# Kernel tuning notes

Measured on AMD Instinct MI355X. Metric: run time of the kernel, lower is better.

The kernel has to match this reference:

```python
import jax, jax.numpy as jnp
import numpy as np

B, T, D, H, L, DFF, MAXLEN = 4, 2048, 512, 8, 6, 2048, 2048
DK = D // H
SCALE = float(1.0 / np.sqrt(DK * 2))  # 1/sqrt(d_k*2)


def layer_norm(x, g, b, eps=1e-5):
    m = jnp.mean(x, axis=-1, keepdims=True)
    v = jnp.var(x, axis=-1, keepdims=True)
    return (x - m) / jnp.sqrt(v + eps) * g + b


def setup_inputs() -> dict:
    key = jax.random.key(0)
    it = iter(jax.random.split(key, 48))
    def n(shape, std=0.02):
        return jax.random.normal(next(it), shape, dtype=jnp.float32) * std
    inp = {}
    inp['x'] = jax.random.normal(next(it), (B, T), dtype=jnp.float32)
    inp['ip_w'] = n((1, D)); inp['ip_b'] = jnp.zeros((D,))
    inp['ip_ln_g'] = jnp.ones((D,)); inp['ip_ln_b'] = jnp.zeros((D,))
    inp['pos_embed'] = n((MAXLEN, D), 0.01)
    inp['pad_token'] = n((D,), 0.01)
    inp['Wq'] = n((L, D, D)); inp['bq'] = jnp.zeros((L, D))
    inp['Wk'] = n((L, D, D)); inp['bk'] = jnp.zeros((L, D))
    inp['Wv'] = n((L, D, D)); inp['bv'] = jnp.zeros((L, D))
    inp['Wo'] = n((L, D, D)); inp['bo'] = jnp.zeros((L, D))
    inp['ln1_g'] = jnp.ones((L, D)); inp['ln1_b'] = jnp.zeros((L, D))
    inp['ln2_g'] = jnp.ones((L, D)); inp['ln2_b'] = jnp.zeros((L, D))
    inp['W1'] = n((L, D, DFF)); inp['b1'] = jnp.zeros((L, DFF))
    inp['W2'] = n((L, DFF, D)); inp['b2'] = jnp.zeros((L, D))
    inp['gate1'] = jnp.full((L,), 0.1); inp['gate2'] = jnp.full((L,), 0.1)
    inp['fn_g'] = jnp.ones((D,)); inp['fn_b'] = jnp.zeros((D,))
    for p in ['bh', 'ah', 'ch']:
        inp[p + '_ln_g'] = jnp.ones((D,)); inp[p + '_ln_b'] = jnp.zeros((D,))
    inp['bh_w'] = n((D, 2), 0.01); inp['bh_b'] = jnp.zeros((2,))
    inp['ah_w'] = n((D, 1), 0.01); inp['ah_b'] = jnp.zeros((1,))
    inp['ch_w'] = n((D, 1), 0.01); inp['ch_b'] = jnp.zeros((1,))
    return inp


def _forward(x, ip_w, ip_b, ip_ln_g, ip_ln_b, pos_embed, pad_token,
             Wq, bq, Wk, bk, Wv, bv, Wo, bo,
             ln1_g, ln1_b, ln2_g, ln2_b, W1, b1, W2, b2, gate1, gate2,
             fn_g, fn_b, bh_ln_g, bh_ln_b, bh_w, bh_b,
             ah_ln_g, ah_ln_b, ah_w, ah_b, ch_ln_g, ch_ln_b, ch_w, ch_b):
    Bx, Tx = x.shape
    xc = jnp.clip(x, -10.0, 10.0)
    pad_mask = xc == -1.0  # [B,T]
    h = layer_norm(xc[..., None] @ ip_w + ip_b, ip_ln_g, ip_ln_b)  # [B,T,D]
    h = h + 0.1 * pos_embed[None, :Tx, :]
    h = jnp.where(pad_mask[..., None], pad_token, h)
    cmask = jnp.triu(jnp.full((Tx, Tx), -10000.0, dtype=h.dtype), k=1)  # additive causal mask
    for i in range(L):
        xn = layer_norm(h, ln1_g[i], ln1_b[i])
        def heads(w, b, xn=xn):
            return (xn @ w + b).reshape(Bx, Tx, H, DK).transpose(0, 2, 1, 3)
        q = heads(Wq[i], bq[i]); k = heads(Wk[i], bk[i]); v = heads(Wv[i], bv[i])
        q = q / jnp.maximum(jnp.linalg.norm(q, axis=-1, keepdims=True), 1e-8)
        k = k / jnp.maximum(jnp.linalg.norm(k, axis=-1, keepdims=True), 1e-8)
        scores = jnp.clip(jnp.einsum('bhtd,bhsd->bhts', q, k) * SCALE, -5.0, 5.0) + cmask
        a = jax.nn.softmax(scores / 1.5, axis=-1)
        o = jnp.einsum('bhts,bhsd->bhtd', a, v).transpose(0, 2, 1, 3).reshape(Bx, Tx, D)
        h = h + gate1[i] * ((o @ Wo[i] + bo[i]) * 0.5)
        xn2 = layer_norm(h, ln2_g[i], ln2_b[i])
        ffn = jax.nn.gelu(xn2 @ W1[i] + b1[i], approximate=False) @ W2[i] + b2[i]
        h = jnp.clip(h + gate2[i] * ffn, -10.0, 10.0)
    h = layer_norm(h, fn_g, fn_b)
    m = (~pad_mask).astype(h.dtype)[..., None]
    mean = (h * m).sum(axis=1) / jnp.maximum(m.sum(axis=1), 1.0)  # masked mean pool [B,D]
    binary = layer_norm(mean, bh_ln_g, bh_ln_b) @ bh_w + bh_b
    anomaly = layer_norm(mean, ah_ln_g, ah_ln_b) @ ah_w + ah_b
    caustic = jax.nn.sigmoid(layer_norm(mean, ch_ln_g, ch_ln_b) @ ch_w + ch_b)
    return jnp.concatenate([binary, anomaly, caustic], axis=-1)  # [B,4]


def reference(x, ip_w, ip_b, ip_ln_g, ip_ln_b, pos_embed, pad_token,
              Wq, bq, Wk, bk, Wv, bv, Wo, bo,
              ln1_g, ln1_b, ln2_g, ln2_b, W1, b1, W2, b2, gate1, gate2,
              fn_g, fn_b, bh_ln_g, bh_ln_b, bh_w, bh_b,
              ah_ln_g, ah_ln_b, ah_w, ah_b, ch_ln_g, ch_ln_b, ch_w, ch_b):
    return _forward(x, ip_w, ip_b, ip_ln_g, ip_ln_b, pos_embed, pad_token,
                    Wq, bq, Wk, bk, Wv, bv, Wo, bo,
                    ln1_g, ln1_b, ln2_g, ln2_b, W1, b1, W2, b2, gate1, gate2,
                    fn_g, fn_b, bh_ln_g, bh_ln_b, bh_w, bh_b,
                    ah_ln_g, ah_ln_b, ah_w, ah_b, ch_ln_g, ch_ln_b, ch_w, ch_b)
```

## Files before the change

kernel.cpp:

```cpp
#include <hip/hip_runtime.h>
#include <hip/hip_bf16.h>
#include <math.h>

constexpr int Bsz = 4, T = 2048, D = 512, H = 8, Lnum = 6, DFF = 2048, DK = 64;
constexpr int QS2 = 1024;
constexpr float K2 = 0.08838834764831845f / 1.5f;

typedef __attribute__((ext_vector_type(8))) short svec8;
typedef __attribute__((ext_vector_type(4))) float fvec4;

__device__ __forceinline__ fvec4 mfma16(svec8 a, svec8 b, fvec4 c) {
    return __builtin_amdgcn_mfma_f32_16x16x32_bf16(a, b, c, 0, 0, 0);
}
__device__ __forceinline__ unsigned short f2b(float f) {
    unsigned int u = __float_as_uint(f);
    u += 0x7fffu + ((u >> 16) & 1u);
    return (unsigned short)(u >> 16);
}
__device__ __forceinline__ unsigned int pk2b(float a, float b) {
    __hip_bfloat162 h = __float22bfloat162_rn(float2{a, b});
    return *(unsigned int*)&h;
}
__device__ __forceinline__ float wave_red_sum(float v) {
    for (int o = 32; o > 0; o >>= 1) v += __shfl_down(v, o, 64);
    return __shfl(v, 0, 64);
}
__device__ __forceinline__ void glds16(const unsigned short* g, unsigned short* l) {
    __builtin_amdgcn_global_load_lds(
        (const __attribute__((address_space(1))) unsigned int*)g,
        (__attribute__((address_space(3))) unsigned int*)l, 16, 0, 0);
}
#define FRAG(buf, row, kq) (*(const svec8*)((buf) + (((row) << 6) | ((((kq) ^ ((row) & 7))) << 3))))

__global__ __launch_bounds__(64)
void embed_kernel(const float* __restrict__ x, const float* __restrict__ ip_w,
                  const float* __restrict__ ip_b, const float* __restrict__ g,
                  const float* __restrict__ bta, const float* __restrict__ pos,
                  const float* __restrict__ pad_tok, float* __restrict__ h)
{
    int row = blockIdx.x;
    int t = row & (T - 1);
    int lane = threadIdx.x;
    float xv = x[row];
    float xc = fminf(fmaxf(xv, -10.f), 10.f);
    bool pad = (xc == -1.0f);
    float pre[8];
    float s = 0.f, s2 = 0.f;
#pragma unroll
    for (int j = 0; j < 8; j++) {
        int d = j * 64 + lane;
        float p = xc * ip_w[d] + ip_b[d];
        pre[j] = p; s += p; s2 += p * p;
    }
    s = wave_red_sum(s); s2 = wave_red_sum(s2);
    float m = s * (1.f / 512.f);
    float var = s2 * (1.f / 512.f) - m * m;
    float rstd = 1.f / sqrtf(var + 1e-5f);
#pragma unroll
    for (int j = 0; j < 8; j++) {
        int d = j * 64 + lane;
        float hv = (pre[j] - m) * rstd * g[d] + bta[d] + 0.1f * pos[(size_t)t * D + d];
        if (pad) hv = pad_tok[d];
        h[(size_t)row * D + d] = hv;
    }
}

__global__ __launch_bounds__(256)
void ln_kernel(const float* __restrict__ in, float* __restrict__ out,
               const float* __restrict__ g, const float* __restrict__ b)
{
    int row = blockIdx.x * 4 + (threadIdx.x >> 6);
    int lane = threadIdx.x & 63;
    const float* r = in + (size_t)row * D;
    float4 v0 = ((const float4*)r)[lane];
    float4 v1 = ((const float4*)r)[lane + 64];
    float s = v0.x + v0.y + v0.z + v0.w + v1.x + v1.y + v1.z + v1.w;
    float s2 = v0.x*v0.x + v0.y*v0.y + v0.z*v0.z + v0.w*v0.w
             + v1.x*v1.x + v1.y*v1.y + v1.z*v1.z + v1.w*v1.w;
    s = wave_red_sum(s); s2 = wave_red_sum(s2);
    float m = s * (1.f / 512.f);
    float var = s2 * (1.f / 512.f) - m * m;
    float rstd = 1.f / sqrtf(var + 1e-5f);
    float4 g0 = ((const float4*)g)[lane], g1 = ((const float4*)g)[lane + 64];
    float4 b0 = ((const float4*)b)[lane], b1 = ((const float4*)b)[lane + 64];
    float4 o0, o1;
    o0.x = (v0.x - m) * rstd * g0.x + b0.x; o0.y = (v0.y - m) * rstd * g0.y + b0.y;
    o0.z = (v0.z - m) * rstd * g0.z + b0.z; o0.w = (v0.w - m) * rstd * g0.w + b0.w;
    o1.x = (v1.x - m) * rstd * g1.x + b1.x; o1.y = (v1.y - m) * rstd * g1.y + b1.y;
    o1.z = (v1.z - m) * rstd * g1.z + b1.z; o1.w = (v1.w - m) * rstd * g1.w + b1.w;
    ((float4*)(out + (size_t)row * D))[lane] = o0;
    ((float4*)(out + (size_t)row * D))[lane + 64] = o1;
}

__device__ __forceinline__ void ln_row_bf16(const float* __restrict__ in, unsigned short* __restrict__ out,
                                            const float* __restrict__ g, const float* __restrict__ b,
                                            int row, int lane)
{
    const float* r = in + (size_t)row * D;
    float4 v0 = ((const float4*)r)[lane];
    float4 v1 = ((const float4*)r)[lane + 64];
    float s = v0.x + v0.y + v0.z + v0.w + v1.x + v1.y + v1.z + v1.w;
    float s2 = v0.x*v0.x + v0.y*v0.y + v0.z*v0.z + v0.w*v0.w
             + v1.x*v1.x + v1.y*v1.y + v1.z*v1.z + v1.w*v1.w;
    s = wave_red_sum(s); s2 = wave_red_sum(s2);
    float m = s * (1.f / 512.f);
    float var = s2 * (1.f / 512.f) - m * m;
    float rstd = 1.f / sqrtf(var + 1e-5f);
    float4 g0 = ((const float4*)g)[lane], g1 = ((const float4*)g)[lane + 64];
    float4 b0 = ((const float4*)b)[lane], b1 = ((const float4*)b)[lane + 64];
    unsigned short o0[4], o1[4];
    o0[0] = f2b((v0.x - m) * rstd * g0.x + b0.x); o0[1] = f2b((v0.y - m) * rstd * g0.y + b0.y);
    o0[2] = f2b((v0.z - m) * rstd * g0.z + b0.z); o0[3] = f2b((v0.w - m) * rstd * g0.w + b0.w);
    o1[0] = f2b((v1.x - m) * rstd * g1.x + b1.x); o1[1] = f2b((v1.y - m) * rstd * g1.y + b1.y);
    o1[2] = f2b((v1.z - m) * rstd * g1.z + b1.z); o1[3] = f2b((v1.w - m) * rstd * g1.w + b1.w);
    *(uint2*)(out + (size_t)row * D + lane * 4) = *(uint2*)o0;
    *(uint2*)(out + (size_t)row * D + 256 + lane * 4) = *(uint2*)o1;
}

__global__ __launch_bounds__(256)
void ln_bf16_kernel(const float* __restrict__ in, unsigned short* __restrict__ out,
                    const float* __restrict__ g, const float* __restrict__ b)
{
    ln_row_bf16(in, out, g, b, blockIdx.x * 4 + (threadIdx.x >> 6), threadIdx.x & 63);
}

__global__ __launch_bounds__(256)
void prep_kernel(const float* __restrict__ wq, const float* __restrict__ wk,
                 const float* __restrict__ wv, const float* __restrict__ wo,
                 const float* __restrict__ w1, const float* __restrict__ w2,
                 unsigned short* __restrict__ oq, unsigned short* __restrict__ ok,
                 unsigned short* __restrict__ ov, unsigned short* __restrict__ oo,
                 unsigned short* __restrict__ o1, unsigned short* __restrict__ o2,
                 const float* __restrict__ hin, unsigned short* __restrict__ lnout,
                 const float* __restrict__ ln_g, const float* __restrict__ ln_b)
{
    __shared__ float tile[32][33];
    int bid = blockIdx.x;
    if (bid >= 3072) {
        int row = (bid - 3072) * 4 + (threadIdx.x >> 6);
        ln_row_bf16(hin, lnout, ln_g, ln_b, row, threadIdx.x & 63);
        return;
    }
    const float* in; unsigned short* out; int K, N, kt, nt;
    if (bid < 1024) {
        int sel = bid >> 8, loc = bid & 255;
        in  = sel == 0 ? wq : sel == 1 ? wk : sel == 2 ? wv : wo;
        out = sel == 0 ? oq : sel == 1 ? ok : sel == 2 ? ov : oo;
        K = 512; N = 512; kt = loc >> 4; nt = loc & 15;
    } else if (bid < 2048) {
        int loc = bid - 1024; in = w1; out = o1; K = 512; N = 2048; kt = loc >> 6; nt = loc & 63;
    } else {
        int loc = bid - 2048; in = w2; out = o2; K = 2048; N = 512; kt = loc >> 4; nt = loc & 15;
    }
    int k0 = kt * 32, n0 = nt * 32;
    int t = threadIdx.x;
    int kr = t >> 3, nc = (t & 7) * 4;
    float4 v = *(const float4*)(in + (size_t)(k0 + kr) * N + n0 + nc);
    tile[kr][nc] = v.x; tile[kr][nc + 1] = v.y; tile[kr][nc + 2] = v.z; tile[kr][nc + 3] = v.w;
    __syncthreads();
    unsigned short o[4];
#pragma unroll
    for (int i = 0; i < 4; i++) o[i] = f2b(tile[nc + i][kr]);
    *(uint2*)(out + (size_t)(n0 + kr) * K + k0 + nc) = *(uint2*)o;
}

template<int EPI, int OBF, int BM>
__global__ __launch_bounds__(256)
void gemm_bf16(const unsigned short* __restrict__ A, const unsigned short* __restrict__ BT,
               const float* __restrict__ bias, const float* __restrict__ bias_b,
               const float* __restrict__ bias_c, const float* __restrict__ res,
               void* __restrict__ Cv, unsigned short* __restrict__ vtout,
               int M, int N, int K, const float* __restrict__ gate_p)
{
    constexpr int WN = (BM == 128) ? 2 : 4;
    constexpr int WSPAN = 128 / WN;
    constexpr int NT = WSPAN / 16;
    constexpr int MT = 4;
    constexpr int ACALLS = BM / 32;
    constexpr int SMEMSZ = (EPI == 0) ? 17408 : (BM * 64 + 128 * 64);
    __shared__ __align__(16) unsigned short SMEM[SMEMSZ];
    unsigned short* As = SMEM;
    unsigned short* Bs = SMEM + BM * 64;
    const int tid = threadIdx.x, w = tid >> 6, lane = tid & 63, quad = lane >> 4, ln = lane & 15;
    const int wm = w / WN, wn = w % WN;
    const int m0 = blockIdx.x * BM, n0 = blockIdx.y * 128;
    const int jg = (lane & 7) ^ ((lane >> 3) & 7);
    const int rb = w * 8 + (lane >> 3);
    const unsigned short* Agl = A + (size_t)(m0 + rb) * K + jg * 8;
    const unsigned short* Bgl = BT + (size_t)(n0 + rb) * K + jg * 8;

    fvec4 acc[MT][NT];
#pragma unroll
    for (int mt = 0; mt < MT; mt++)
#pragma unroll
        for (int nt = 0; nt < NT; nt++)
#pragma unroll
            for (int r = 0; r < 4; r++) acc[mt][nt][r] = 0.f;

    for (int k0 = 0; k0 < K; k0 += 64) {
        __syncthreads();
#pragma unroll
        for (int c = 0; c < ACALLS; c++)
            glds16(Agl + k0 + (size_t)c * 32 * K, As + c * 2048 + w * 512);
#pragma unroll
        for (int c = 0; c < 4; c++)
            glds16(Bgl + k0 + (size_t)c * 32 * K, Bs + c * 2048 + w * 512);
        __syncthreads();
#pragma unroll
        for (int kk = 0; kk < 2; kk++) {
            svec8 af[MT], bfr[NT];
#pragma unroll
            for (int mt = 0; mt < MT; mt++)
                af[mt] = FRAG(As, wm * 64 + mt * 16 + ln, kk * 4 + quad);
#pragma unroll
            for (int nt = 0; nt < NT; nt++)
                bfr[nt] = FRAG(Bs, wn * WSPAN + nt * 16 + ln, kk * 4 + quad);
#pragma unroll
            for (int mt = 0; mt < MT; mt++)
#pragma unroll
                for (int nt = 0; nt < NT; nt++)
                    acc[mt][nt] = mfma16(af[mt], bfr[nt], acc[mt][nt]);
        }
    }

    const float gate = (EPI == 1 || EPI == 3) ? gate_p[0] : 0.f;
    float bb[NT];
#pragma unroll
    for (int nt = 0; nt < NT; nt++) {
        int n = n0 + wn * WSPAN + nt * 16 + ln;
        if (EPI == 0) {
            int nseg = n >> 9;
            const float* bsel = nseg == 0 ? bias : (nseg == 1 ? bias_b : bias_c);
            bb[nt] = bsel[n - nseg * 512];
        } else {
            bb[nt] = bias[n];
        }
    }

    if (EPI == 0 && n0 >= 1024) {
        __syncthreads();
#pragma unroll
        for (int mt = 0; mt < MT; mt++) {
#pragma unroll
            for (int nt = 0; nt < NT; nt++) {
                int nl = wn * 64 + nt * 16 + ln;
                int mb = wm * 64 + mt * 16 + quad * 4;
                unsigned int lo = pk2b(acc[mt][nt][0] + bb[nt], acc[mt][nt][1] + bb[nt]);
                unsigned int hi = pk2b(acc[mt][nt][2] + bb[nt], acc[mt][nt][3] + bb[nt]);
                uint2 u; u.x = lo; u.y = hi;
                *(uint2*)(SMEM + nl * 136 + mb) = u;
            }
        }
        __syncthreads();
        int row = tid >> 1, half = (tid & 1) * 64;
        unsigned short* dst = vtout + ((size_t)((m0 >> 11) * 512 + (n0 - 1024) + row)) * T
                              + (m0 & (T - 1)) + half;
        const unsigned short* src = SMEM + row * 136 + half;
#pragma unroll
        for (int j = 0; j < 8; j++) *(uint4*)(dst + j * 8) = *(const uint4*)(src + j * 8);
        return;
    }

#pragma unroll
    for (int mt = 0; mt < MT; mt++) {
        float v[NT][4];
#pragma unroll
        for (int nt = 0; nt < NT; nt++)
#pragma unroll
            for (int r = 0; r < 4; r++) v[nt][r] = acc[mt][nt][r] + bb[nt];
        if (EPI == 0) {
            const float fac = ((n0 + wn * WSPAN) < 512) ? K2 : 1.f;
#pragma unroll
            for (int r = 0; r < 4; r++) {
                float s = 0.f;
#pragma unroll
                for (int nt = 0; nt < NT; nt++) s += v[nt][r] * v[nt][r];
                s += __shfl_xor(s, 1); s += __shfl_xor(s, 2);
                s += __shfl_xor(s, 4); s += __shfl_xor(s, 8);
                float rs = fac / fmaxf(sqrtf(s), 1e-8f);
#pragma unroll
                for (int nt = 0; nt < NT; nt++) v[nt][r] *= rs;
            }
        }
#pragma unroll
        for (int nt = 0; nt < NT; nt++) {
            int n = n0 + wn * WSPAN + nt * 16 + ln;
#pragma unroll
            for (int r = 0; r < 4; r++) {
                int m = m0 + wm * 64 + mt * 16 + quad * 4 + r;
                float val = v[nt][r];
                if (EPI == 0) {
                    ((unsigned short*)Cv)[(size_t)m * QS2 + n] = f2b(val);
                } else {
                    size_t off = (size_t)m * N + n;
                    if (EPI == 1) val = res[off] + gate * 0.5f * val;
                    else if (EPI == 2) {
                        float u = val;
                        float z = 0.7978845608028654f * fmaf(0.044715f * u, u * u, u);
                        float e = __builtin_amdgcn_exp2f(z * 2.8853900817779268f);
                        float rr = __builtin_amdgcn_rcpf(e + 1.f);
                        val = u * (1.f - rr);
                    }
                    else if (EPI == 3) val = fminf(fmaxf(res[off] + gate * val, -10.f), 10.f);
                    if (OBF) ((unsigned short*)Cv)[off] = f2b(val);
                    else ((float*)Cv)[off] = val;
                }
            }
        }
    }
}

template<bool MERGED, bool DIAGS>
__device__ __forceinline__ void attn_step2(
    unsigned short* PsA, unsigned short* PsB,
    const unsigned short* Ks, const unsigned short* Vt,
    svec8 qA0, svec8 qA1, svec8 qB0, svec8 qB1,
    bool diagA, bool diagB,
    fvec4 (&oA)[4], fvec4& lA, fvec4 (&oB)[4], fvec4& lB,
    int w, int quad, int ln)
{
    constexpr short BONE = (short)0x3F80;
    const svec8 ONES8 = {BONE, BONE, BONE, BONE, BONE, BONE, BONE, BONE};
    const int qrow = w * 16 + ln;
    const int prow_base = (qrow << 6);
#pragma unroll
    for (int nt = 0; nt < 4; nt++) {
        svec8 kf0 = FRAG(Ks, nt * 16 + ln, quad);
        svec8 kf1 = FRAG(Ks, nt * 16 + ln, 4 + quad);
        const int sbase = nt * 16 + quad * 4;
        const int paddr = prow_base | ((((sbase >> 3) ^ (qrow & 7))) << 3) | (sbase & 7);
        {
            fvec4 z; z[0] = z[1] = z[2] = z[3] = 0.f;
            z = mfma16(kf0, qB0, z);
            z = mfma16(kf1, qB1, z);
            float p[4];
#pragma unroll
            for (int r = 0; r < 4; r++) {
                float y = z[r];
                float pv = fmaf(y, fmaf(y, 0.5f, 1.f), 1.f);
                if (DIAGS && diagB && (sbase + r > qrow)) pv = 0.f;
                p[r] = pv;
            }
            uint2 u; u.x = pk2b(p[0], p[1]); u.y = pk2b(p[2], p[3]);
            *(uint2*)(PsB + paddr) = u;
        }
        if (MERGED) {
            fvec4 z; z[0] = z[1] = z[2] = z[3] = 0.f;
            z = mfma16(kf0, qA0, z);
            z = mfma16(kf1, qA1, z);
            float p[4];
#pragma unroll
            for (int r = 0; r < 4; r++) {
                float y = z[r];
                float pv = fmaf(y, fmaf(y, 0.5f, 1.f), 1.f);
                if (DIAGS && diagA && (sbase + r > qrow)) pv = 0.f;
                p[r] = pv;
            }
            uint2 u; u.x = pk2b(p[0], p[1]); u.y = pk2b(p[2], p[3]);
            *(uint2*)(PsA + paddr) = u;
        }
    }
#pragma unroll
    for (int ks = 0; ks < 2; ks++) {
        svec8 paB = FRAG(PsB, w * 16 + ln, ks * 4 + quad);
        lB = mfma16(paB, ONES8, lB);
        svec8 paA;
        if (MERGED) { paA = FRAG(PsA, w * 16 + ln, ks * 4 + quad); lA = mfma16(paA, ONES8, lA); }
#pragma unroll
        for (int nt = 0; nt < 4; nt++) {
            svec8 vf = FRAG(Vt, nt * 16 + ln, ks * 4 + quad);
            oB[nt] = mfma16(paB, vf, oB[nt]);
            if (MERGED) oA[nt] = mfma16(paA, vf, oA[nt]);
        }
    }
}

__device__ __forceinline__ void attn_do_step(
    int s, int p, int nst,
    unsigned short* PsA, unsigned short* PsB,
    const unsigned short* Ks, const unsigned short* Vt,
    svec8 qA0, svec8 qA1, svec8 qB0, svec8 qB1,
    fvec4 (&oA)[4], fvec4& lA, fvec4 (&oB)[4], fvec4& lB,
    int w, int quad, int ln)
{
    const bool doA = (s <= p), dA = (s == p), dB = (s == nst - 1);
    if (doA) {
        if (dA | dB) attn_step2<true , true >(PsA, PsB, Ks, Vt, qA0, qA1, qB0, qB1, dA, dB, oA, lA, oB, lB, w, quad, ln);
        else         attn_step2<true , false>(PsA, PsB, Ks, Vt, qA0, qA1, qB0, qB1, dA, dB, oA, lA, oB, lB, w, quad, ln);
    } else {
        if (dB)      attn_step2<false, true >(PsA, PsB, Ks, Vt, qA0, qA1, qB0, qB1, dA, dB, oA, lA, oB, lB, w, quad, ln);
        else         attn_step2<false, false>(PsA, PsB, Ks, Vt, qA0, qA1, qB0, qB1, dA, dB, oA, lA, oB, lB, w, quad, ln);
    }
}

__global__ __launch_bounds__(256)
void attn_pair_kernel(const unsigned short* __restrict__ qkv, const unsigned short* __restrict__ vt,
                      unsigned short* __restrict__ o)
{
    __shared__ __align__(16) unsigned short PsA[4096], PsB[4096];
    __shared__ __align__(16) unsigned short Kb[4][4096], Vb[4][4096];
    const int fid = blockIdx.x;
    const int xcd = fid & 7, slot = fid >> 3;
    const int bh = xcd * 4 + (slot & 3);
    const int p = slot >> 2;
    const int b = bh >> 3, hh = bh & 7;
    const int qtA = p, qtB = 31 - p, nst = 32 - p;
    const int tid = threadIdx.x, w = tid >> 6, lane = tid & 63, quad = lane >> 4, ln = lane & 15;
    const int rl = lane >> 3, sl = lane & 7, jgz = sl ^ rl;
    const int w8 = w * 8;
    const int grow = w8 + rl;
    const unsigned short* qrow_p = qkv + ((size_t)(b * T) + grow) * QS2 + hh * 64 + jgz * 8;
    const unsigned short* krow_p = qrow_p + 512;
    const unsigned short* vrow_p = vt + ((size_t)(bh * 64) + grow) * T + jgz * 8;

    glds16(qrow_p + (size_t)(qtA * 64) * QS2, PsA + w8 * 64);
    glds16(qrow_p + (size_t)(qtA * 64 + 32) * QS2, PsA + (w8 + 32) * 64);
    glds16(qrow_p + (size_t)(qtB * 64) * QS2, PsB + w8 * 64);
    glds16(qrow_p + (size_t)(qtB * 64 + 32) * QS2, PsB + (w8 + 32) * 64);

    svec8 qA0 = {}, qA1 = {}, qB0 = {}, qB1 = {};
    fvec4 oA[4], oB[4], lAv, lBv;
#pragma unroll
    for (int r = 0; r < 4; r++) { lAv[r] = 0.f; lBv[r] = 0.f; }
#pragma unroll
    for (int nt = 0; nt < 4; nt++)
#pragma unroll
        for (int r = 0; r < 4; r++) { oA[nt][r] = 0.f; oB[nt][r] = 0.f; }

    const int Nph = (nst + 3) >> 2;
    for (int ph = 0; ph < Nph; ph++) {
        const int sb = 4 * ph;
        __syncthreads();
#pragma unroll
        for (int i = 0; i < 4; i++) {
            const int s = sb + i;
            if (s < nst) {
                glds16(krow_p + (size_t)(s * 64) * QS2, Kb[i] + w8 * 64);
                glds16(krow_p + (size_t)(s * 64 + 32) * QS2, Kb[i] + (w8 + 32) * 64);
                glds16(vrow_p + s * 64, Vb[i] + w8 * 64);
                glds16(vrow_p + (size_t)32 * T + s * 64, Vb[i] + (w8 + 32) * 64);
            }
        }
        __syncthreads();
        if (ph == 0) {
            qA0 = FRAG(PsA, w * 16 + ln, quad); qA1 = FRAG(PsA, w * 16 + ln, 4 + quad);
            qB0 = FRAG(PsB, w * 16 + ln, quad); qB1 = FRAG(PsB, w * 16 + ln, 4 + quad);
        }
#pragma unroll
        for (int i = 0; i < 4; i++) {
            const int s = sb + i;
            if (s < nst)
                attn_do_step(s, p, nst, PsA, PsB, Kb[i], Vb[i],
                             qA0, qA1, qB0, qB1, oA, lAv, oB, lBv, w, quad, ln);
        }
    }

    unsigned short* ogA = o + (size_t)(b * T + qtA * 64 + w * 16 + quad * 4) * D + hh * 64;
    unsigned short* ogB = o + (size_t)(b * T + qtB * 64 + w * 16 + quad * 4) * D + hh * 64;
#pragma unroll
    for (int r = 0; r < 4; r++) {
        float ia = 1.f / lAv[r], ib = 1.f / lBv[r];
#pragma unroll
        for (int nt = 0; nt < 4; nt++) {
            ogA[(size_t)r * D + nt * 16 + ln] = f2b(oA[nt][r] * ia);
            ogB[(size_t)r * D + nt * 16 + ln] = f2b(oB[nt][r] * ib);
        }
    }
}

__global__ __launch_bounds__(256)
void pool_kernel(const float* __restrict__ hn, const float* __restrict__ x, float* __restrict__ part)
{
    int b = blockIdx.x, ch = blockIdx.y, tid = threadIdx.x;
    int t0 = ch * 128;
    float s0 = 0.f, s1 = 0.f, cnt = 0.f;
    for (int tt = 0; tt < 128; tt++) {
        int t = t0 + tt;
        float xv = x[b * T + t];
        float m = (xv == -1.0f) ? 0.f : 1.f;
        cnt += m;
        const float* r = hn + ((size_t)(b * T + t)) * D;
        s0 += r[tid] * m;
        s1 += r[tid + 256] * m;
    }
    float* pr = part + (size_t)(b * 16 + ch) * 513;
    pr[tid] = s0; pr[tid + 256] = s1;
    if (tid == 0) pr[512] = cnt;
}

__global__ __launch_bounds__(64)
void head_kernel(const float* __restrict__ part,
                 const float* __restrict__ bh_g, const float* __restrict__ bh_bl,
                 const float* __restrict__ ah_g, const float* __restrict__ ah_bl,
                 const float* __restrict__ ch_g, const float* __restrict__ ch_bl,
                 const float* __restrict__ bh_w, const float* __restrict__ bh_b2,
                 const float* __restrict__ ah_w, const float* __restrict__ ah_b2,
                 const float* __restrict__ ch_w, const float* __restrict__ ch_b2,
                 float* __restrict__ out)
{
    int b = blockIdx.x, lane = threadIdx.x;
    float cnt = 0.f;
    for (int c = 0; c < 16; c++) cnt += part[(size_t)(b * 16 + c) * 513 + 512];
    float denom = fmaxf(cnt, 1.f);
    float md[8];
    float s = 0.f, s2 = 0.f;
#pragma unroll
    for (int j = 0; j < 8; j++) {
        int d = j * 64 + lane;
        float acc = 0.f;
        for (int c = 0; c < 16; c++) acc += part[(size_t)(b * 16 + c) * 513 + d];
        md[j] = acc / denom;
        s += md[j]; s2 += md[j] * md[j];
    }
    s = wave_red_sum(s); s2 = wave_red_sum(s2);
    float mu = s * (1.f / 512.f);
    float var = s2 * (1.f / 512.f) - mu * mu;
    float rstd = 1.f / sqrtf(var + 1e-5f);
    float a0 = 0.f, a1 = 0.f, a2 = 0.f, a3 = 0.f;
#pragma unroll
    for (int j = 0; j < 8; j++) {
        int d = j * 64 + lane;
        float z = (md[j] - mu) * rstd;
        float zb = z * bh_g[d] + bh_bl[d];
        a0 += zb * bh_w[d * 2 + 0];
        a1 += zb * bh_w[d * 2 + 1];
        a2 += (z * ah_g[d] + ah_bl[d]) * ah_w[d];
        a3 += (z * ch_g[d] + ch_bl[d]) * ch_w[d];
    }
    a0 = wave_red_sum(a0); a1 = wave_red_sum(a1);
    a2 = wave_red_sum(a2); a3 = wave_red_sum(a3);
    if (lane == 0) {
        out[b * 4 + 0] = a0 + bh_b2[0];
        out[b * 4 + 1] = a1 + bh_b2[1];
        out[b * 4 + 2] = a2 + ah_b2[0];
        float t3 = a3 + ch_b2[0];
        out[b * 4 + 3] = 1.f / (1.f + expf(-t3));
    }
}

extern "C" void kernel_launch(void* const* d_in, const int* in_sizes, int n_in,
                              void* d_out, int out_size, void* d_ws, size_t ws_size,
                              hipStream_t stream)
{
    const float* x      = (const float*)d_in[0];
    const float* ip_w   = (const float*)d_in[1];
    const float* ip_b   = (const float*)d_in[2];
    const float* ip_ln_g= (const float*)d_in[3];
    const float* ip_ln_b= (const float*)d_in[4];
    const float* pos    = (const float*)d_in[5];
    const float* pad_tok= (const float*)d_in[6];
    const float* Wq = (const float*)d_in[7];  const float* bq = (const float*)d_in[8];
    const float* Wk = (const float*)d_in[9];  const float* bk = (const float*)d_in[10];
    const float* Wv = (const float*)d_in[11]; const float* bv = (const float*)d_in[12];
    const float* Wo = (const float*)d_in[13]; const float* bo = (const float*)d_in[14];
    const float* ln1_g = (const float*)d_in[15]; const float* ln1_b = (const float*)d_in[16];
    const float* ln2_g = (const float*)d_in[17]; const float* ln2_b = (const float*)d_in[18];
    const float* W1 = (const float*)d_in[19]; const float* b1 = (const float*)d_in[20];
    const float* W2 = (const float*)d_in[21]; const float* b2 = (const float*)d_in[22];
    const float* gate1 = (const float*)d_in[23]; const float* gate2 = (const float*)d_in[24];
    const float* fn_g = (const float*)d_in[25]; const float* fn_b = (const float*)d_in[26];
    const float* bh_g  = (const float*)d_in[27]; const float* bh_bl = (const float*)d_in[28];
    const float* ah_g  = (const float*)d_in[29]; const float* ah_bl = (const float*)d_in[30];
    const float* ch_g  = (const float*)d_in[31]; const float* ch_bl = (const float*)d_in[32];
    const float* bh_w  = (const float*)d_in[33]; const float* bh_b2 = (const float*)d_in[34];
    const float* ah_w  = (const float*)d_in[35]; const float* ah_b2 = (const float*)d_in[36];
    const float* ch_w  = (const float*)d_in[37]; const float* ch_b2 = (const float*)d_in[38];

    char* ws = (char*)d_ws;
    float*          h     = (float*)ws;
    unsigned short* act_b = (unsigned short*)(ws + 16777216);
    unsigned short* qkv   = (unsigned short*)(ws + 25165824);
    unsigned short* mid_b = (unsigned short*)(ws + 41943040);
    float*          xn_f  = (float*)(ws + 41943040);
    unsigned short* wT    = (unsigned short*)(ws + 75497472);
    unsigned short* vt    = (unsigned short*)(ws + 81788928);
    float*          part  = (float*)(ws + 90177536);
    float*          out   = (float*)d_out;

    unsigned short* wqT = wT;
    unsigned short* wkT = wT + 262144;
    unsigned short* wvT = wT + 524288;
    unsigned short* woT = wT + 786432;
    unsigned short* w1T = wT + 1048576;
    unsigned short* w2T = wT + 2097152;

    embed_kernel<<<dim3(Bsz * T), dim3(64), 0, stream>>>(x, ip_w, ip_b, ip_ln_g, ip_ln_b, pos, pad_tok, h);

    for (int i = 0; i < Lnum; i++) {
        const size_t dd = (size_t)i * D * D;
        const size_t df = (size_t)i * D * DFF;
        prep_kernel<<<dim3(5120), dim3(256), 0, stream>>>(Wq + dd, Wk + dd, Wv + dd, Wo + dd,
                                                          W1 + df, W2 + df,
                                                          wqT, wkT, wvT, woT, w1T, w2T,
                                                          h, act_b, ln1_g + i * D, ln1_b + i * D);
        gemm_bf16<0, 1, 128><<<dim3(64, 12), dim3(256), 0, stream>>>(act_b, wqT, bq + i * D, bk + i * D, bv + i * D,
                                                                     nullptr, qkv, vt, Bsz * T, 1536, D, nullptr);
        attn_pair_kernel<<<dim3(512), dim3(256), 0, stream>>>(qkv, vt, act_b);
        gemm_bf16<1, 0, 64><<<dim3(128, 4), dim3(256), 0, stream>>>(act_b, woT, bo + i * D, nullptr, nullptr,
                                                                    h, h, nullptr, Bsz * T, D, D, gate1 + i);
        ln_bf16_kernel<<<dim3(Bsz * T / 4), dim3(256), 0, stream>>>(h, act_b, ln2_g + i * D, ln2_b + i * D);
        gemm_bf16<2, 1, 128><<<dim3(64, 16), dim3(256), 0, stream>>>(act_b, w1T, b1 + i * DFF, nullptr, nullptr,
                                                                     nullptr, mid_b, nullptr, Bsz * T, DFF, D, nullptr);
        gemm_bf16<3, 0, 64><<<dim3(128, 4), dim3(256), 0, stream>>>(mid_b, w2T, b2 + i * D, nullptr, nullptr,
                                                                    h, h, nullptr, Bsz * T, D, DFF, gate2 + i);
    }

    ln_kernel<<<dim3(Bsz * T / 4), dim3(256), 0, stream>>>(h, xn_f, fn_g, fn_b);
    pool_kernel<<<dim3(Bsz, 16), dim3(256), 0, stream>>>(xn_f, x, part);
    head_kernel<<<dim3(Bsz), dim3(64), 0, stream>>>(part, bh_g, bh_bl, ah_g, ah_bl, ch_g, ch_bl,
                                                    bh_w, bh_b2, ah_w, ah_b2, ch_w, ch_b2, out);
}
```

Measured before the change: 1.132 ms.

## Restructure attention to one query tile per block with key-split waves

Replaces the paired-query-tile attention kernel (4 waves, 256 threads, shared K/V staging with block barriers) with a kernel where each 128-thread block handles one 64-row query tile. Its two waves split the key tiles between them, each streaming its own double-buffered K/V via per-wave async LDS loads and vmcnt waits instead of __syncthreads. Partial outputs and row sums are reduced through LDS at the end. Block order interleaves short and long causal tiles to balance load. This removes block-wide barriers and raises MFMA work per loaded K/V tile, at the cost of more registers per wave (16 accumulators plus Q fragments), an extra reduction pass, and twice as many blocks.

```diff
diff --git a/kernel.cpp b/kernel.cpp
--- a/kernel.cpp
+++ b/kernel.cpp
@@ -30,6 +30,7 @@
         (const __attribute__((address_space(1))) unsigned int*)g,
         (__attribute__((address_space(3))) unsigned int*)l, 16, 0, 0);
 }
+#define WAITVM(n) __builtin_amdgcn_s_waitcnt(0x0F70 | ((n) & 0xF) | ((((n) >> 4) & 3) << 14))
 #define FRAG(buf, row, kq) (*(const svec8*)((buf) + (((row) << 6) | ((((kq) ^ ((row) & 7))) << 3))))
 
 __global__ __launch_bounds__(64)
@@ -310,160 +311,149 @@
     }
 }
 
-template<bool MERGED, bool DIAGS>
-__device__ __forceinline__ void attn_step2(
-    unsigned short* PsA, unsigned short* PsB,
-    const unsigned short* Ks, const unsigned short* Vt,
-    svec8 qA0, svec8 qA1, svec8 qB0, svec8 qB1,
-    bool diagA, bool diagB,
-    fvec4 (&oA)[4], fvec4& lA, fvec4 (&oB)[4], fvec4& lB,
-    int w, int quad, int ln)
+template<bool DIAG>
+__device__ __forceinline__ void attn_step64(
+    unsigned short* Psw, const unsigned short* Ks, const unsigned short* Vt,
+    const svec8 (&qf)[4][2], fvec4 (&oacc)[4][4], fvec4 (&lacc)[4],
+    int quad, int ln)
 {
     constexpr short BONE = (short)0x3F80;
     const svec8 ONES8 = {BONE, BONE, BONE, BONE, BONE, BONE, BONE, BONE};
-    const int qrow = w * 16 + ln;
-    const int prow_base = (qrow << 6);
 #pragma unroll
     for (int nt = 0; nt < 4; nt++) {
         svec8 kf0 = FRAG(Ks, nt * 16 + ln, quad);
         svec8 kf1 = FRAG(Ks, nt * 16 + ln, 4 + quad);
         const int sbase = nt * 16 + quad * 4;
-        const int paddr = prow_base | ((((sbase >> 3) ^ (qrow & 7))) << 3) | (sbase & 7);
-        {
+#pragma unroll
+        for (int qg = 0; qg < 4; qg++) {
             fvec4 z; z[0] = z[1] = z[2] = z[3] = 0.f;
-            z = mfma16(kf0, qB0, z);
-            z = mfma16(kf1, qB1, z);
+            z = mfma16(kf0, qf[qg][0], z);
+            z = mfma16(kf1, qf[qg][1], z);
+            const int qcol = qg * 16 + ln;
             float p[4];
 #pragma unroll
             for (int r = 0; r < 4; r++) {
                 float y = z[r];
                 float pv = fmaf(y, fmaf(y, 0.5f, 1.f), 1.f);
-                if (DIAGS && diagB && (sbase + r > qrow)) pv = 0.f;
+                if (DIAG && (sbase + r > qcol)) pv = 0.f;
                 p[r] = pv;
             }
             uint2 u; u.x = pk2b(p[0], p[1]); u.y = pk2b(p[2], p[3]);
-            *(uint2*)(PsB + paddr) = u;
-        }
-        if (MERGED) {
-            fvec4 z; z[0] = z[1] = z[2] = z[3] = 0.f;
-            z = mfma16(kf0, qA0, z);
-            z = mfma16(kf1, qA1, z);
-            float p[4];
-#pragma unroll
-            for (int r = 0; r < 4; r++) {
-                float y = z[r];
-                float pv = fmaf(y, fmaf(y, 0.5f, 1.f), 1.f);
-                if (DIAGS && diagA && (sbase + r > qrow)) pv = 0.f;
-                p[r] = pv;
+            const int paddr = (qcol << 6) | ((((sbase >> 3) ^ (qcol & 7))) << 3) | (sbase & 7);
+            *(uint2*)(Psw + paddr) = u;
+        }
+    }
+#pragma unroll
+    for (int ks = 0; ks < 2; ks++) {
+        svec8 pa[4];
+#pragma unroll
+        for (int qm = 0; qm < 4; qm++) {
+            pa[qm] = FRAG(Psw, qm * 16 + ln, ks * 4 + quad);
+            lacc[qm] = mfma16(pa[qm], ONES8, lacc[qm]);
+        }
+#pragma unroll
+        for (int dkn = 0; dkn < 4; dkn++) {
+            svec8 vf = FRAG(Vt, dkn * 16 + ln, ks * 4 + quad);
+#pragma unroll
+            for (int qm = 0; qm < 4; qm++)
+                oacc[qm][dkn] = mfma16(pa[qm], vf, oacc[qm][dkn]);
+        }
+    }
+}
+
+__global__ __launch_bounds__(128)
+void attn_kernel(const unsigned short* __restrict__ qkv, const unsigned short* __restrict__ vt,
+                 unsigned short* __restrict__ o)
+{
+    __shared__ __align__(16) unsigned short Kb[2][2][4096];
+    __shared__ __align__(16) unsigned short Vb[2][2][4096];
+    __shared__ __align__(16) unsigned short Ps[2][4096];
+    const int fid = blockIdx.x;
+    const int c = fid & 255, slot = fid >> 8, k = c >> 5;
+    const int bh = c & 31;
+    const int qt = (slot == 0) ? k : (slot == 1) ? 15 - k : (slot == 2) ? 16 + k : 31 - k;
+    const int b = bh >> 3, hh = bh & 7;
+    const int nst = qt + 1;
+    const int tid = threadIdx.x, w = tid >> 6, lane = tid & 63, quad = lane >> 4, ln = lane & 15;
+    const int jgz = (lane & 7) ^ (lane >> 3);
+
+    svec8 qf[4][2];
+#pragma unroll
+    for (int qg = 0; qg < 4; qg++) {
+        const unsigned short* qp = qkv + ((size_t)(b * T + qt * 64 + qg * 16 + ln)) * QS2 + hh * 64;
+        qf[qg][0] = *(const svec8*)(qp + quad * 8);
+        qf[qg][1] = *(const svec8*)(qp + 32 + quad * 8);
+    }
+
+    const unsigned short* kbase = qkv + ((size_t)(b * T) + (lane >> 3)) * QS2 + 512 + hh * 64 + jgz * 8;
+    const unsigned short* vbase = vt + ((size_t)(bh * 64) + (lane >> 3)) * T + jgz * 8;
+
+    fvec4 oacc[4][4], lacc[4];
+#pragma unroll
+    for (int qm = 0; qm < 4; qm++) {
+#pragma unroll
+        for (int r = 0; r < 4; r++) lacc[qm][r] = 0.f;
+#pragma unroll
+        for (int dkn = 0; dkn < 4; dkn++)
+#pragma unroll
+            for (int r = 0; r < 4; r++) oacc[qm][dkn][r] = 0.f;
+    }
+
+    if (w < nst) {
+#pragma unroll
+        for (int cc = 0; cc < 8; cc++) {
+            glds16(kbase + ((size_t)(w * 64) + cc * 8) * QS2, Kb[w][0] + cc * 512);
+            glds16(vbase + (size_t)(cc * 8) * T + w * 64, Vb[w][0] + cc * 512);
+        }
+        int buf = 0;
+        for (int s = w; s < nst; s += 2, buf ^= 1) {
+            const int snext = s + 2;
+            const bool pre = (snext < nst);
+            if (pre) {
+#pragma unroll
+                for (int cc = 0; cc < 8; cc++) {
+                    glds16(kbase + ((size_t)(snext * 64) + cc * 8) * QS2, Kb[w][buf ^ 1] + cc * 512);
+                    glds16(vbase + (size_t)(cc * 8) * T + snext * 64, Vb[w][buf ^ 1] + cc * 512);
+                }
+                WAITVM(16);
+            } else {
+                WAITVM(0);
             }
-            uint2 u; u.x = pk2b(p[0], p[1]); u.y = pk2b(p[2], p[3]);
-            *(uint2*)(PsA + paddr) = u;
-        }
-    }
-#pragma unroll
-    for (int ks = 0; ks < 2; ks++) {
-        svec8 paB = FRAG(PsB, w * 16 + ln, ks * 4 + quad);
-        lB = mfma16(paB, ONES8, lB);
-        svec8 paA;
-        if (MERGED) { paA = FRAG(PsA, w * 16 + ln, ks * 4 + quad); lA = mfma16(paA, ONES8, lA); }
-#pragma unroll
-        for (int nt = 0; nt < 4; nt++) {
-            svec8 vf = FRAG(Vt, nt * 16 + ln, ks * 4 + quad);
-            oB[nt] = mfma16(paB, vf, oB[nt]);
-            if (MERGED) oA[nt] = mfma16(paA, vf, oA[nt]);
-        }
-    }
-}
-
-__device__ __forceinline__ void attn_do_step(
-    int s, int p, int nst,
-    unsigned short* PsA, unsigned short* PsB,
-    const unsigned short* Ks, const unsigned short* Vt,
-    svec8 qA0, svec8 qA1, svec8 qB0, svec8 qB1,
-    fvec4 (&oA)[4], fvec4& lA, fvec4 (&oB)[4], fvec4& lB,
-    int w, int quad, int ln)
-{
-    const bool doA = (s <= p), dA = (s == p), dB = (s == nst - 1);
-    if (doA) {
-        if (dA | dB) attn_step2<true , true >(PsA, PsB, Ks, Vt, qA0, qA1, qB0, qB1, dA, dB, oA, lA, oB, lB, w, quad, ln);
-        else         attn_step2<true , false>(PsA, PsB, Ks, Vt, qA0, qA1, qB0, qB1, dA, dB, oA, lA, oB, lB, w, quad, ln);
-    } else {
-        if (dB)      attn_step2<false, true >(PsA, PsB, Ks, Vt, qA0, qA1, qB0, qB1, dA, dB, oA, lA, oB, lB, w, quad, ln);
-        else         attn_step2<false, false>(PsA, PsB, Ks, Vt, qA0, qA1, qB0, qB1, dA, dB, oA, lA, oB, lB, w, quad, ln);
-    }
-}
-
-__global__ __launch_bounds__(256)
-void attn_pair_kernel(const unsigned short* __restrict__ qkv, const unsigned short* __restrict__ vt,
-                      unsigned short* __restrict__ o)
-{
-    __shared__ __align__(16) unsigned short PsA[4096], PsB[4096];
-    __shared__ __align__(16) unsigned short Kb[4][4096], Vb[4][4096];
-    const int fid = blockIdx.x;
-    const int xcd = fid & 7, slot = fid >> 3;
-    const int bh = xcd * 4 + (slot & 3);
-    const int p = slot >> 2;
-    const int b = bh >> 3, hh = bh & 7;
-    const int qtA = p, qtB = 31 - p, nst = 32 - p;
-    const int tid = threadIdx.x, w = tid >> 6, lane = tid & 63, quad = lane >> 4, ln = lane & 15;
-    const int rl = lane >> 3, sl = lane & 7, jgz = sl ^ rl;
-    const int w8 = w * 8;
-    const int grow = w8 + rl;
-    const unsigned short* qrow_p = qkv + ((size_t)(b * T) + grow) * QS2 + hh * 64 + jgz * 8;
-    const unsigned short* krow_p = qrow_p + 512;
-    const unsigned short* vrow_p = vt + ((size_t)(bh * 64) + grow) * T + jgz * 8;
-
-    glds16(qrow_p + (size_t)(qtA * 64) * QS2, PsA + w8 * 64);
-    glds16(qrow_p + (size_t)(qtA * 64 + 32) * QS2, PsA + (w8 + 32) * 64);
-    glds16(qrow_p + (size_t)(qtB * 64) * QS2, PsB + w8 * 64);
-    glds16(qrow_p + (size_t)(qtB * 64 + 32) * QS2, PsB + (w8 + 32) * 64);
-
-    svec8 qA0 = {}, qA1 = {}, qB0 = {}, qB1 = {};
-    fvec4 oA[4], oB[4], lAv, lBv;
-#pragma unroll
-    for (int r = 0; r < 4; r++) { lAv[r] = 0.f; lBv[r] = 0.f; }
-#pragma unroll
-    for (int nt = 0; nt < 4; nt++)
-#pragma unroll
-        for (int r = 0; r < 4; r++) { oA[nt][r] = 0.f; oB[nt][r] = 0.f; }
-
-    const int Nph = (nst + 3) >> 2;
-    for (int ph = 0; ph < Nph; ph++) {
-        const int sb = 4 * ph;
-        __syncthreads();
-#pragma unroll
-        for (int i = 0; i < 4; i++) {
-            const int s = sb + i;
-            if (s < nst) {
-                glds16(krow_p + (size_t)(s * 64) * QS2, Kb[i] + w8 * 64);
-                glds16(krow_p + (size_t)(s * 64 + 32) * QS2, Kb[i] + (w8 + 32) * 64);
-                glds16(vrow_p + s * 64, Vb[i] + w8 * 64);
-                glds16(vrow_p + (size_t)32 * T + s * 64, Vb[i] + (w8 + 32) * 64);
+            __builtin_amdgcn_sched_barrier(0);
+            if (s == qt) attn_step64<true >(Ps[w], Kb[w][buf], Vb[w][buf], qf, oacc, lacc, quad, ln);
+            else         attn_step64<false>(Ps[w], Kb[w][buf], Vb[w][buf], qf, oacc, lacc, quad, ln);
+        }
+    }
+
+    __syncthreads();
+    float* red = (float*)&Kb[0][0][0];
+    float* mine = red + w * 5120 + lane * 80;
+#pragma unroll
+    for (int qm = 0; qm < 4; qm++) {
+#pragma unroll
+        for (int dkn = 0; dkn < 4; dkn++)
+#pragma unroll
+            for (int r = 0; r < 4; r++) mine[qm * 16 + dkn * 4 + r] = oacc[qm][dkn][r];
+#pragma unroll
+        for (int r = 0; r < 4; r++) mine[64 + qm * 4 + r] = lacc[qm][r];
+    }
+    __syncthreads();
+    const float* other = red + (w ^ 1) * 5120 + lane * 80;
+#pragma unroll
+    for (int half = 0; half < 2; half++) {
+        const int qm = w * 2 + half;
+        float lsum[4];
+#pragma unroll
+        for (int r = 0; r < 4; r++) lsum[r] = lacc[qm][r] + other[64 + qm * 4 + r];
+        unsigned short* og = o + (size_t)(b * T + qt * 64 + qm * 16 + quad * 4) * D + hh * 64;
+#pragma unroll
+        for (int r = 0; r < 4; r++) {
+            float inv = 1.f / lsum[r];
+#pragma unroll
+            for (int dkn = 0; dkn < 4; dkn++) {
+                float osum = oacc[qm][dkn][r] + other[qm * 16 + dkn * 4 + r];
+                og[(size_t)r * D + dkn * 16 + ln] = f2b(osum * inv);
             }
-        }
-        __syncthreads();
-        if (ph == 0) {
-            qA0 = FRAG(PsA, w * 16 + ln, quad); qA1 = FRAG(PsA, w * 16 + ln, 4 + quad);
-            qB0 = FRAG(PsB, w * 16 + ln, quad); qB1 = FRAG(PsB, w * 16 + ln, 4 + quad);
-        }
-#pragma unroll
-        for (int i = 0; i < 4; i++) {
-            const int s = sb + i;
-            if (s < nst)
-                attn_do_step(s, p, nst, PsA, PsB, Kb[i], Vb[i],
-                             qA0, qA1, qB0, qB1, oA, lAv, oB, lBv, w, quad, ln);
-        }
-    }
-
-    unsigned short* ogA = o + (size_t)(b * T + qtA * 64 + w * 16 + quad * 4) * D + hh * 64;
-    unsigned short* ogB = o + (size_t)(b * T + qtB * 64 + w * 16 + quad * 4) * D + hh * 64;
-#pragma unroll
-    for (int r = 0; r < 4; r++) {
-        float ia = 1.f / lAv[r], ib = 1.f / lBv[r];
-#pragma unroll
-        for (int nt = 0; nt < 4; nt++) {
-            ogA[(size_t)r * D + nt * 16 + ln] = f2b(oA[nt][r] * ia);
-            ogB[(size_t)r * D + nt * 16 + ln] = f2b(oB[nt][r] * ib);
         }
     }
 }
@@ -595,7 +585,7 @@
                                                           h, act_b, ln1_g + i * D, ln1_b + i * D);
         gemm_bf16<0, 1, 128><<<dim3(64, 12), dim3(256), 0, stream>>>(act_b, wqT, bq + i * D, bk + i * D, bv + i * D,
                                                                      nullptr, qkv, vt, Bsz * T, 1536, D, nullptr);
-        attn_pair_kernel<<<dim3(512), dim3(256), 0, stream>>>(qkv, vt, act_b);
+        attn_kernel<<<dim3(1024), dim3(128), 0, stream>>>(qkv, vt, act_b);
         gemm_bf16<1, 0, 64><<<dim3(128, 4), dim3(256), 0, stream>>>(act_b, woT, bo + i * D, nullptr, nullptr,
                                                                     h, h, nullptr, Bsz * T, D, D, gate1 + i);
         ln_bf16_kernel<<<dim3(Bsz * T / 4), dim3(256), 0, stream>>>(h, act_b, ln2_g + i * D, ln2_b + i * D);
```

New measurement: 1.315 ms. 1.16x slower.
